# Optimization experiments

Hardware: AMD Instinct MI355X
Metric: run time of the kernel (lower is better)

Reference implementation:

```python
import jax, jax.numpy as jnp
import numpy as np
from jax import lax

HIDDEN = 1024
MEM = 32      # memory slots M
KEY = 32      # key dim
VAL = 32      # value dim
DECAY = 0.85
TAU = 0.5
WARMUP = 4
B = 2048
T = 64        # number of recurrent steps


def setup_inputs() -> dict:
    key = jax.random.key(0)
    ks = jax.random.split(key, 5)
    s = 0.02  # nn.init.normal_(w, 0, 0.02)
    return {
        "h": jax.random.normal(ks[0], (B, T, HIDDEN), jnp.float32),
        "W_gate": jax.random.normal(ks[1], (1, HIDDEN), jnp.float32) * s,
        "b_gate": jnp.zeros((1,), jnp.float32),
        "W_query": jax.random.normal(ks[2], (KEY, HIDDEN), jnp.float32) * s,
        "b_query": jnp.zeros((KEY,), jnp.float32),
        "W_fk": jax.random.normal(ks[3], (KEY, HIDDEN), jnp.float32) * s,
        "b_fk": jnp.zeros((KEY,), jnp.float32),
        "W_fv": jax.random.normal(ks[4], (VAL, HIDDEN), jnp.float32) * s,
        "b_fv": jnp.zeros((VAL,), jnp.float32),
    }


def reference(h, W_gate, b_gate, W_query, b_query, W_fk, b_fk, W_fv, b_fv):
    Bsz = h.shape[0]
    scale = 1.0 / (KEY ** 0.5)

    def step(carry, h_t):
        K, V, Tf, mask, step_i = carry  # K:(B,M,KEY) V:(B,M,VAL) Tf,mask:(B,M)
        p_reuse = jax.nn.sigmoid(h_t @ W_gate.T + b_gate)[:, 0]        # (B,)
        q = h_t @ W_query.T + b_query                                   # (B,KEY)
        fk = h_t @ W_fk.T + b_fk                                        # (B,KEY)
        fv = h_t @ W_fv.T + b_fv                                        # (B,VAL)
        # masked attention read over memory slots
        logits = jnp.einsum('bmk,bk->bm', K, q) * scale                 # (B,M)
        attn = jax.nn.softmax(logits + (1.0 - mask) * -1e9, axis=-1)    # (B,M)
        retrv = jnp.einsum('bm,bmv->bv', attn, V)                       # (B,VAL)
        empty_row = (jnp.sum(mask, axis=-1) == 0).astype(h_t.dtype)     # (B,)
        warm = jnp.where(step_i < WARMUP, 1.0, 0.0).astype(h_t.dtype)   # scalar
        gate = p_reuse * (1.0 - empty_row) * (1.0 - warm)               # (B,)
        e_t = gate[:, None] * retrv + (1.0 - gate)[:, None] * fv        # (B,VAL)
        # eviction + one-hot scatter write
        write = jnp.logical_or(gate < TAU, warm > 0).astype(h_t.dtype)  # (B,)
        evict_idx = jnp.argmin(Tf + mask * 0.001, axis=-1)              # (B,)
        idx_oh = jax.nn.one_hot(evict_idx, MEM, dtype=K.dtype)          # (B,M)
        write_w = write[:, None] * idx_oh                               # (B,M)
        w3 = write_w[:, :, None]
        K_new = K * (1.0 - w3) + w3 * fk[:, None, :]
        V_new = V * (1.0 - w3) + w3 * fv[:, None, :]
        # freshness EMA bump
        reuse_oh = jax.nn.one_hot(jnp.argmax(attn, axis=-1), MEM, dtype=Tf.dtype)
        bump_w = write[:, None] * idx_oh + (1.0 - write)[:, None] * reuse_oh
        T_new = Tf * DECAY + bump_w * (1.0 - Tf * DECAY)
        mask_new = jnp.minimum(mask + write_w, 1.0)
        return (K_new, V_new, T_new, mask_new, step_i + 1), (e_t, p_reuse)

    carry0 = (
        jnp.zeros((Bsz, MEM, KEY), h.dtype),
        jnp.zeros((Bsz, MEM, VAL), h.dtype),
        jnp.zeros((Bsz, MEM), h.dtype),
        jnp.zeros((Bsz, MEM), h.dtype),
        jnp.int32(0),
    )
    _, (es, ps) = lax.scan(step, carry0, jnp.swapaxes(h, 0, 1))
    # es: (T,B,VAL) -> (B,T,VAL); ps: (T,B) -> (B,T)
    return jnp.swapaxes(es, 0, 1), jnp.swapaxes(ps, 0, 1)
```

## Files before the change

### kernel.cpp

```cpp
#include <hip/hip_runtime.h>
#include <cmath>

#define BSZ   2048
#define TSTEP 64
#define HDIM  1024
#define RTOT  (BSZ * TSTEP)
#define MEMN  32

constexpr int BM = 128, BN = 128, BK = 32;

__global__ __launch_bounds__(256) void proj_kernel(
    const float* __restrict__ h,
    const float* __restrict__ Wg,  const float* __restrict__ bg,
    const float* __restrict__ Wq,  const float* __restrict__ bq,
    const float* __restrict__ Wfk, const float* __restrict__ bfk,
    const float* __restrict__ Wfv, const float* __restrict__ bfv,
    float* __restrict__ G, float* __restrict__ Qo,
    float* __restrict__ FKo, float* __restrict__ FVo)
{
    __shared__ __align__(16) float Xs[BK][BM + 4];
    __shared__ __align__(16) float Ws[BK][BN];

    const int tid  = threadIdx.x;
    const int tx   = tid & 15;
    const int ty   = tid >> 4;
    const int row0 = blockIdx.x * BM;

    float acc[8][8];
#pragma unroll
    for (int i = 0; i < 8; ++i)
#pragma unroll
        for (int j = 0; j < 8; ++j) acc[i][j] = 0.f;

    for (int k0 = 0; k0 < HDIM; k0 += BK) {
#pragma unroll
        for (int it = 0; it < 4; ++it) {
            int task = tid + it * 256;
            int rr   = task >> 3;
            int kv   = (task & 7) << 2;
            const float4 xv = *reinterpret_cast<const float4*>(
                &h[(size_t)(row0 + rr) * HDIM + k0 + kv]);
            Xs[kv + 0][rr] = xv.x;
            Xs[kv + 1][rr] = xv.y;
            Xs[kv + 2][rr] = xv.z;
            Xs[kv + 3][rr] = xv.w;
        }
#pragma unroll
        for (int it = 0; it < 4; ++it) {
            int task = tid + it * 256;
            int nn   = task >> 3;
            int kv   = (task & 7) << 2;
            float4 wv = make_float4(0.f, 0.f, 0.f, 0.f);
            const float* src = nullptr;
            if (nn < 32)       src = Wq  + (size_t)nn * HDIM;
            else if (nn < 64)  src = Wfk + (size_t)(nn - 32) * HDIM;
            else if (nn < 96)  src = Wfv + (size_t)(nn - 64) * HDIM;
            else if (nn == 96) src = Wg;
            if (src) wv = *reinterpret_cast<const float4*>(&src[k0 + kv]);
            Ws[kv + 0][nn] = wv.x;
            Ws[kv + 1][nn] = wv.y;
            Ws[kv + 2][nn] = wv.z;
            Ws[kv + 3][nn] = wv.w;
        }
        __syncthreads();

#pragma unroll
        for (int k = 0; k < BK; ++k) {
            const float4 a0 = *reinterpret_cast<const float4*>(&Xs[k][ty * 4]);
            const float4 a1 = *reinterpret_cast<const float4*>(&Xs[k][64 + ty * 4]);
            const float4 b0 = *reinterpret_cast<const float4*>(&Ws[k][tx * 4]);
            const float4 b1 = *reinterpret_cast<const float4*>(&Ws[k][64 + tx * 4]);
            const float av[8] = {a0.x, a0.y, a0.z, a0.w, a1.x, a1.y, a1.z, a1.w};
            const float bv[8] = {b0.x, b0.y, b0.z, b0.w, b1.x, b1.y, b1.z, b1.w};
#pragma unroll
            for (int i = 0; i < 8; ++i)
#pragma unroll
                for (int j = 0; j < 8; ++j)
                    acc[i][j] = fmaf(av[i], bv[j], acc[i][j]);
        }
        __syncthreads();
    }

#pragma unroll
    for (int i = 0; i < 8; ++i) {
        const int rl = (i < 4) ? (ty * 4 + i) : (64 + ty * 4 + (i - 4));
        const size_t r = (size_t)row0 + rl;
#pragma unroll
        for (int j = 0; j < 8; ++j) {
            const int c = (j < 4) ? (tx * 4 + j) : (64 + tx * 4 + (j - 4));
            const float v = acc[i][j];
            if (c < 32)        Qo [r * 32 + c]        = v + bq[c];
            else if (c < 64)   FKo[r * 32 + (c - 32)] = v + bfk[c - 32];
            else if (c < 96)   FVo[r * 32 + (c - 64)] = v + bfv[c - 64];
            else if (c == 96) {
                const float x = v + bg[0];
                G[r] = 1.f / (1.f + expf(-x));
            }
        }
    }
}

__global__ __launch_bounds__(128) void recur_kernel(
    const float* __restrict__ G,  const float* __restrict__ Qp,
    const float* __restrict__ FKp, const float* __restrict__ FVp,
    float* __restrict__ out)
{
    __shared__ float Ks[4][MEMN][33];
    __shared__ float Vs[4][MEMN][33];
    __shared__ float qs[4][MEMN];
    __shared__ float attn_s[4][MEMN];

    const int tid = threadIdx.x;
    const int el  = tid >> 5;
    const int m   = tid & 31;
    const size_t b = (size_t)blockIdx.x * 4 + el;

#pragma unroll
    for (int k = 0; k < MEMN; ++k) { Ks[el][m][k] = 0.f; Vs[el][m][k] = 0.f; }
    float Tf  = 0.f;
    float msk = 0.f;
    __syncthreads();

    const float scale = 0.17677669529663687f;
    float* es_out = out;
    float* ps_out = out + (size_t)RTOT * 32;

    for (int t = 0; t < TSTEP; ++t) {
        const size_t r = b * TSTEP + t;
        const float q  = Qp [r * 32 + m];
        const float fk = FKp[r * 32 + m];
        const float fv = FVp[r * 32 + m];
        const float p  = G[r];

        qs[el][m] = q;
        __syncthreads();

        float accv = 0.f;
#pragma unroll
        for (int k = 0; k < MEMN; ++k) accv = fmaf(Ks[el][m][k], qs[el][k], accv);
        const float lg = accv * scale + (1.f - msk) * (-1e9f);

        float mx = lg;
#pragma unroll
        for (int d = 16; d >= 1; d >>= 1) mx = fmaxf(mx, __shfl_xor(mx, d));
        const float pe = expf(lg - mx);
        float ssum = pe;
#pragma unroll
        for (int d = 16; d >= 1; d >>= 1) ssum += __shfl_xor(ssum, d);
        const float attn = pe / ssum;
        attn_s[el][m] = attn;

        float smk = msk;
#pragma unroll
        for (int d = 16; d >= 1; d >>= 1) smk += __shfl_xor(smk, d);

        float av = attn; int ai = m;
#pragma unroll
        for (int d = 16; d >= 1; d >>= 1) {
            const float ov = __shfl_xor(av, d);
            const int   oi = __shfl_xor(ai, d);
            if (ov > av || (ov == av && oi < ai)) { av = ov; ai = oi; }
        }
        float evv = Tf + msk * 0.001f; int ei = m;
#pragma unroll
        for (int d = 16; d >= 1; d >>= 1) {
            const float ov = __shfl_xor(evv, d);
            const int   oi = __shfl_xor(ei, d);
            if (ov < evv || (ov == evv && oi < ei)) { evv = ov; ei = oi; }
        }
        __syncthreads();

        float rv = 0.f;
#pragma unroll
        for (int k = 0; k < MEMN; ++k) rv = fmaf(attn_s[el][k], Vs[el][k][m], rv);

        const float empty = (smk == 0.f) ? 1.f : 0.f;
        const float warm  = (t < 4) ? 1.f : 0.f;
        const float gate  = p * (1.f - empty) * (1.f - warm);
        const float e_val = gate * rv + (1.f - gate) * fv;

        es_out[r * 32 + m] = e_val;
        if (m == 0) ps_out[r] = p;

        const bool wr = (gate < 0.5f) || (warm > 0.f);
        __syncthreads();

        if (wr) { Ks[el][ei][m] = fk; Vs[el][ei][m] = fv; }

        const float x = Tf * 0.85f;
        const bool bump = wr ? (m == ei) : (m == ai);
        Tf = bump ? (x + (1.f - x)) : x;
        if (wr && m == ei) msk = 1.f;
        __syncthreads();
    }
}

extern "C" void kernel_launch(void* const* d_in, const int* in_sizes, int n_in,
                              void* d_out, int out_size, void* d_ws, size_t ws_size,
                              hipStream_t stream) {
    const float* h   = (const float*)d_in[0];
    const float* Wg  = (const float*)d_in[1];
    const float* bg  = (const float*)d_in[2];
    const float* Wq  = (const float*)d_in[3];
    const float* bq  = (const float*)d_in[4];
    const float* Wfk = (const float*)d_in[5];
    const float* bfk = (const float*)d_in[6];
    const float* Wfv = (const float*)d_in[7];
    const float* bfv = (const float*)d_in[8];

    float* G   = (float*)d_ws;
    float* Qp  = G + RTOT;
    float* FKp = Qp + (size_t)RTOT * 32;
    float* FVp = FKp + (size_t)RTOT * 32;

    proj_kernel<<<RTOT / BM, 256, 0, stream>>>(h, Wg, bg, Wq, bq, Wfk, bfk,
                                               Wfv, bfv, G, Qp, FKp, FVp);
    recur_kernel<<<BSZ / 4, 128, 0, stream>>>(G, Qp, FKp, FVp, (float*)d_out);
}
```

Before: 1.180 ms.

## Enlarge projection GEMM tile and prefetch next-step inputs in recurrence loop

The projection GEMM tile grows to 256 rows with a 16x8 per-thread micro-tile. Each thread now loads one full row slice of h, and the weight shared-memory array is padded. The recurrence kernel prefetches the next timestep's q/fk/fv/gate values into registers while the current step runs. It also replaces __syncthreads with a barrier that waits only on LDS counters, and drops the trailing barrier, so global loads can stay in flight across steps. In exchange the GEMM uses more registers per thread, and the new per-thread row loads are strided across threads, which may hurt coalescing.

New measurement: 1.103 ms. 6.6% less time.

```diff
diff --git a/kernel.cpp b/kernel.cpp
--- a/kernel.cpp
+++ b/kernel.cpp
@@ -7,9 +7,9 @@
 #define RTOT  (BSZ * TSTEP)
 #define MEMN  32
 
-constexpr int BM = 128, BN = 128, BK = 32;
-
-__global__ __launch_bounds__(256) void proj_kernel(
+constexpr int BM = 256, BN = 128, BK = 32;
+
+__global__ __launch_bounds__(256, 2) void proj_kernel(
     const float* __restrict__ h,
     const float* __restrict__ Wg,  const float* __restrict__ bg,
     const float* __restrict__ Wq,  const float* __restrict__ bq,
@@ -19,61 +19,60 @@
     float* __restrict__ FKo, float* __restrict__ FVo)
 {
     __shared__ __align__(16) float Xs[BK][BM + 4];
-    __shared__ __align__(16) float Ws[BK][BN];
+    __shared__ __align__(16) float Ws[BK][BN + 4];
 
     const int tid  = threadIdx.x;
     const int tx   = tid & 15;
     const int ty   = tid >> 4;
     const int row0 = blockIdx.x * BM;
 
-    float acc[8][8];
-#pragma unroll
-    for (int i = 0; i < 8; ++i)
-#pragma unroll
-        for (int j = 0; j < 8; ++j) acc[i][j] = 0.f;
+    float acc[16][8] = {};
 
     for (int k0 = 0; k0 < HDIM; k0 += BK) {
+        {
+            const float* src = &h[(size_t)(row0 + tid) * HDIM + k0];
+#pragma unroll
+            for (int q = 0; q < 8; ++q) {
+                const float4 v = *reinterpret_cast<const float4*>(src + q * 4);
+                Xs[q * 4 + 0][tid] = v.x;
+                Xs[q * 4 + 1][tid] = v.y;
+                Xs[q * 4 + 2][tid] = v.z;
+                Xs[q * 4 + 3][tid] = v.w;
+            }
+        }
 #pragma unroll
         for (int it = 0; it < 4; ++it) {
-            int task = tid + it * 256;
-            int rr   = task >> 3;
-            int kv   = (task & 7) << 2;
-            const float4 xv = *reinterpret_cast<const float4*>(
-                &h[(size_t)(row0 + rr) * HDIM + k0 + kv]);
-            Xs[kv + 0][rr] = xv.x;
-            Xs[kv + 1][rr] = xv.y;
-            Xs[kv + 2][rr] = xv.z;
-            Xs[kv + 3][rr] = xv.w;
-        }
-#pragma unroll
-        for (int it = 0; it < 4; ++it) {
-            int task = tid + it * 256;
-            int nn   = task >> 3;
-            int kv   = (task & 7) << 2;
+            const int task = tid + it * 256;
+            const int nn   = task & 127;
+            const int kq   = task >> 7;
             float4 wv = make_float4(0.f, 0.f, 0.f, 0.f);
             const float* src = nullptr;
             if (nn < 32)       src = Wq  + (size_t)nn * HDIM;
             else if (nn < 64)  src = Wfk + (size_t)(nn - 32) * HDIM;
             else if (nn < 96)  src = Wfv + (size_t)(nn - 64) * HDIM;
             else if (nn == 96) src = Wg;
-            if (src) wv = *reinterpret_cast<const float4*>(&src[k0 + kv]);
-            Ws[kv + 0][nn] = wv.x;
-            Ws[kv + 1][nn] = wv.y;
-            Ws[kv + 2][nn] = wv.z;
-            Ws[kv + 3][nn] = wv.w;
+            if (src) wv = *reinterpret_cast<const float4*>(&src[k0 + kq * 4]);
+            Ws[kq * 4 + 0][nn] = wv.x;
+            Ws[kq * 4 + 1][nn] = wv.y;
+            Ws[kq * 4 + 2][nn] = wv.z;
+            Ws[kq * 4 + 3][nn] = wv.w;
         }
         __syncthreads();
 
-#pragma unroll
         for (int k = 0; k < BK; ++k) {
-            const float4 a0 = *reinterpret_cast<const float4*>(&Xs[k][ty * 4]);
-            const float4 a1 = *reinterpret_cast<const float4*>(&Xs[k][64 + ty * 4]);
+            float av[16], bv[8];
+#pragma unroll
+            for (int g = 0; g < 4; ++g) {
+                const float4 a = *reinterpret_cast<const float4*>(&Xs[k][g * 64 + ty * 4]);
+                av[g * 4 + 0] = a.x; av[g * 4 + 1] = a.y;
+                av[g * 4 + 2] = a.z; av[g * 4 + 3] = a.w;
+            }
             const float4 b0 = *reinterpret_cast<const float4*>(&Ws[k][tx * 4]);
             const float4 b1 = *reinterpret_cast<const float4*>(&Ws[k][64 + tx * 4]);
-            const float av[8] = {a0.x, a0.y, a0.z, a0.w, a1.x, a1.y, a1.z, a1.w};
-            const float bv[8] = {b0.x, b0.y, b0.z, b0.w, b1.x, b1.y, b1.z, b1.w};
-#pragma unroll
-            for (int i = 0; i < 8; ++i)
+            bv[0] = b0.x; bv[1] = b0.y; bv[2] = b0.z; bv[3] = b0.w;
+            bv[4] = b1.x; bv[5] = b1.y; bv[6] = b1.z; bv[7] = b1.w;
+#pragma unroll
+            for (int i = 0; i < 16; ++i)
 #pragma unroll
                 for (int j = 0; j < 8; ++j)
                     acc[i][j] = fmaf(av[i], bv[j], acc[i][j]);
@@ -82,8 +81,8 @@
     }
 
 #pragma unroll
-    for (int i = 0; i < 8; ++i) {
-        const int rl = (i < 4) ? (ty * 4 + i) : (64 + ty * 4 + (i - 4));
+    for (int i = 0; i < 16; ++i) {
+        const int rl = (i >> 2) * 64 + ty * 4 + (i & 3);
         const size_t r = (size_t)row0 + rl;
 #pragma unroll
         for (int j = 0; j < 8; ++j) {
@@ -100,6 +99,10 @@
     }
 }
 
+__device__ __forceinline__ void lds_barrier() {
+    asm volatile("s_waitcnt lgkmcnt(0)\n\ts_barrier" ::: "memory");
+}
+
 __global__ __launch_bounds__(128) void recur_kernel(
     const float* __restrict__ G,  const float* __restrict__ Qp,
     const float* __restrict__ FKp, const float* __restrict__ FVp,
@@ -125,15 +128,21 @@
     float* es_out = out;
     float* ps_out = out + (size_t)RTOT * 32;
 
+    size_t r = b * TSTEP;
+    float q  = Qp [r * 32 + m];
+    float fk = FKp[r * 32 + m];
+    float fv = FVp[r * 32 + m];
+    float p  = G[r];
+
     for (int t = 0; t < TSTEP; ++t) {
-        const size_t r = b * TSTEP + t;
-        const float q  = Qp [r * 32 + m];
-        const float fk = FKp[r * 32 + m];
-        const float fv = FVp[r * 32 + m];
-        const float p  = G[r];
+        const size_t rn = r + ((t < TSTEP - 1) ? 1 : 0);
+        const float qn  = Qp [rn * 32 + m];
+        const float fkn = FKp[rn * 32 + m];
+        const float fvn = FVp[rn * 32 + m];
+        const float pn  = G[rn];
 
         qs[el][m] = q;
-        __syncthreads();
+        lds_barrier();
 
         float accv = 0.f;
 #pragma unroll
@@ -168,7 +177,7 @@
             const int   oi = __shfl_xor(ei, d);
             if (ov < evv || (ov == evv && oi < ei)) { evv = ov; ei = oi; }
         }
-        __syncthreads();
+        lds_barrier();
 
         float rv = 0.f;
 #pragma unroll
@@ -183,7 +192,7 @@
         if (m == 0) ps_out[r] = p;
 
         const bool wr = (gate < 0.5f) || (warm > 0.f);
-        __syncthreads();
+        lds_barrier();
 
         if (wr) { Ks[el][ei][m] = fk; Vs[el][ei][m] = fv; }
 
@@ -191,7 +200,8 @@
         const bool bump = wr ? (m == ei) : (m == ai);
         Tf = bump ? (x + (1.f - x)) : x;
         if (wr && m == ei) msk = 1.f;
-        __syncthreads();
+
+        q = qn; fk = fkn; fv = fvn; p = pn; r = rn;
     }
 }
 
```
